# Performance work log

Measured on AMD Instinct MI355X. Metric: run time of the kernel, lower is better.

Reference implementation:

```python
import jax, jax.numpy as jnp
import numpy as np

B, S, H, DK = 4, 2048, 16, 64
D = H * DK  # d_model = 1024


def setup_inputs() -> dict:
    key = jax.random.key(0)
    ks = jax.random.split(key, 11)
    s = 1.0 / np.sqrt(D)
    return {
        "query": jax.random.normal(ks[0], (B, S, D), dtype=jnp.float32),
        "value": jax.random.normal(ks[1], (B, S, D), dtype=jnp.float32),
        "key": jax.random.normal(ks[2], (B, S, D), dtype=jnp.float32),
        "Wq": jax.random.normal(ks[3], (D, D), dtype=jnp.float32) * s,
        "bq": jnp.zeros((D,), dtype=jnp.float32),
        "Wk": jax.random.normal(ks[4], (D, D), dtype=jnp.float32) * s,
        "bk": jnp.zeros((D,), dtype=jnp.float32),
        "Wv": jax.random.normal(ks[5], (D, D), dtype=jnp.float32) * s,
        "bv": jnp.zeros((D,), dtype=jnp.float32),
        "Wo": jax.random.normal(ks[6], (D, D), dtype=jnp.float32) * s,
        "bo": jnp.zeros((D,), dtype=jnp.float32),
    }


def _split_heads(x):
    # [B, S, D] -> [B, H, S, DK]
    return x.reshape(B, -1, H, DK).transpose(0, 2, 1, 3)


def reference(query, value, key, Wq, bq, Wk, bk, Wv, bv, Wo, bo):
    q = _split_heads(query @ Wq + bq)
    k = _split_heads(key @ Wk + bk)
    v = _split_heads(value @ Wv + bv)
    logits = jnp.einsum("bhqd,bhkd->bhqk", q, k) / jnp.sqrt(jnp.float32(DK))
    attn = jax.nn.softmax(logits, axis=-1)
    out = jnp.einsum("bhqk,bhkd->bhqd", attn, v)  # [B, H, S, DK]
    out = out.transpose(0, 2, 1, 3).reshape(B, -1, D)
    return out @ Wo + bo
```

## Files before the change

kernel.cpp:

```cpp
#include <hip/hip_runtime.h>

typedef unsigned short u16;
typedef __attribute__((ext_vector_type(4))) short short4v;
typedef __attribute__((ext_vector_type(8))) short short8;
typedef __attribute__((ext_vector_type(4))) float f32x4;

#define MB_ (1024 * 1024)

__device__ __forceinline__ u16 f2bf(float f) {
  union { float f; unsigned int u; } v; v.f = f;
  unsigned int r = (v.u + 0x7FFFu + ((v.u >> 16) & 1u)) >> 16;
  return (u16)r;
}

__device__ __forceinline__ void async16(const void* g, void* l) {
  __builtin_amdgcn_global_load_lds((__attribute__((address_space(1))) void*)g,
                                   (__attribute__((address_space(3))) void*)l, 16, 0, 0);
}

__device__ __forceinline__ f32x4 mfma32(short8 a, short8 b, f32x4 c) {
  return __builtin_amdgcn_mfma_f32_16x16x32_bf16(a, b, c, 0, 0, 0);
}

__global__ void cvt_x(const float* __restrict__ a, const float* __restrict__ b,
                      const float* __restrict__ c, u16* __restrict__ oa,
                      u16* __restrict__ ob, u16* __restrict__ oc) {
  const float* s = blockIdx.y == 0 ? a : (blockIdx.y == 1 ? b : c);
  u16* d = blockIdx.y == 0 ? oa : (blockIdx.y == 1 ? ob : oc);
  size_t i = ((size_t)blockIdx.x * 256 + threadIdx.x) * 4;
  float4 f = *(const float4*)&s[i];
  ushort4 o;
  o.x = f2bf(f.x); o.y = f2bf(f.y); o.z = f2bf(f.z); o.w = f2bf(f.w);
  *(ushort4*)&d[i] = o;
}

__global__ void wtrans(const float* __restrict__ w0, const float* __restrict__ w1,
                       const float* __restrict__ w2, const float* __restrict__ w3,
                       u16* __restrict__ o0, u16* __restrict__ o1,
                       u16* __restrict__ o2, u16* __restrict__ o3) {
  const int z = blockIdx.z;
  const float* in = z == 0 ? w0 : (z == 1 ? w1 : (z == 2 ? w2 : w3));
  u16* out = z == 0 ? o0 : (z == 1 ? o1 : (z == 2 ? o2 : o3));
  __shared__ float tile[32][33];
  const int bx = blockIdx.x * 32, by = blockIdx.y * 32;
  for (int i = threadIdx.y; i < 32; i += 8)
    tile[i][threadIdx.x] = in[(size_t)(by + i) * 1024 + bx + threadIdx.x];
  __syncthreads();
  for (int i = threadIdx.y; i < 32; i += 8)
    out[(size_t)(bx + i) * 1024 + by + threadIdx.x] = f2bf(tile[threadIdx.x][i]);
}

template <int MODE>
__device__ __forceinline__ void gemm_body(const u16* __restrict__ A, const u16* __restrict__ Bt,
                                          const float* __restrict__ bias, float alpha,
                                          void* __restrict__ outp) {
  __shared__ __align__(16) u16 As[128 * 32];
  __shared__ __align__(16) u16 Bs[128 * 32];
  const int t = threadIdx.x, wave = t >> 6, lane = t & 63;
  const int m0 = blockIdx.y * 128, n0 = blockIdx.x * 128;
  const int wm = (wave >> 1) * 64, wn = (wave & 1) * 64;
  const int lrow = lane >> 2, lcol = (lane & 3) * 8;
  f32x4 acc[4][4] = {};
  for (int k0 = 0; k0 < 1024; k0 += 32) {
    __syncthreads();
#pragma unroll
    for (int c = 0; c < 2; ++c) {
      const int chunk = wave * 2 + c;
      const int row = chunk * 16 + lrow;
      async16(&A[(size_t)(m0 + row) * 1024 + k0 + lcol], &As[chunk * 512]);
      async16(&Bt[(size_t)(n0 + row) * 1024 + k0 + lcol], &Bs[chunk * 512]);
    }
    __syncthreads();
    short8 af[4], bf[4];
#pragma unroll
    for (int mb = 0; mb < 4; ++mb)
      af[mb] = *(const short8*)&As[(wm + mb * 16 + (lane & 15)) * 32 + (lane >> 4) * 8];
#pragma unroll
    for (int nb = 0; nb < 4; ++nb)
      bf[nb] = *(const short8*)&Bs[(wn + nb * 16 + (lane & 15)) * 32 + (lane >> 4) * 8];
#pragma unroll
    for (int mb = 0; mb < 4; ++mb)
#pragma unroll
      for (int nb = 0; nb < 4; ++nb)
        acc[mb][nb] = mfma32(af[mb], bf[nb], acc[mb][nb]);
  }
#pragma unroll
  for (int mb = 0; mb < 4; ++mb)
#pragma unroll
    for (int nb = 0; nb < 4; ++nb) {
      const int n = n0 + wn + nb * 16 + (lane & 15);
      const float bn = bias[n];
      if (MODE == 2) {
        const int h = n >> 6, d = n & 63;
        const int mbase = m0 + wm + mb * 16 + (lane >> 4) * 4;
        const int b = mbase >> 11, s = mbase & 2047;
        ushort4 pk;
        pk.x = f2bf(acc[mb][nb][0] + bn);
        pk.y = f2bf(acc[mb][nb][1] + bn);
        pk.z = f2bf(acc[mb][nb][2] + bn);
        pk.w = f2bf(acc[mb][nb][3] + bn);
        *(ushort4*)&((u16*)outp)[(size_t)((b * 16 + h) * 64 + d) * 2048 + s] = pk;
      } else {
#pragma unroll
        for (int r = 0; r < 4; ++r) {
          const int m = m0 + wm + mb * 16 + (lane >> 4) * 4 + r;
          const float v = (acc[mb][nb][r] + bn) * alpha;
          if (MODE == 1) {
            const int b = m >> 11, s = m & 2047, h = n >> 6, d = n & 63;
            ((u16*)outp)[(size_t)((b * 16 + h) * 2048 + s) * 64 + d] = f2bf(v);
          } else {
            ((float*)outp)[(size_t)m * 1024 + n] = v;
          }
        }
      }
    }
}

__global__ __launch_bounds__(256, 2) void gemm_projqk(
    const u16* xq, const u16* xk, const u16* wq, const u16* wk,
    const float* bq, const float* bk, u16* oq, u16* ok, float aq) {
  const int z = blockIdx.z;
  gemm_body<1>(z == 0 ? xq : xk, z == 0 ? wq : wk, z == 0 ? bq : bk,
               z == 0 ? aq : 1.0f, z == 0 ? (void*)oq : (void*)ok);
}

__global__ __launch_bounds__(256, 2) void gemm_projv(const u16* xv, const u16* wv,
                                                     const float* bv, u16* ov) {
  gemm_body<2>(xv, wv, bv, 1.0f, ov);
}

__global__ __launch_bounds__(256, 2) void gemm_out(const u16* A, const u16* Bt,
                                                   const float* bias, float* o) {
  gemm_body<0>(A, Bt, bias, 1.0f, o);
}

__global__ __launch_bounds__(256, 4) void flash_attn(const u16* __restrict__ Q,
                                                     const u16* __restrict__ K,
                                                     const u16* __restrict__ Vt,
                                                     u16* __restrict__ O) {
  __shared__ __align__(16) u16 lds[2 * 64 * 64];
  u16* Ks = lds;
  u16* Vs = lds + 4096;
  const int t = threadIdx.x, wave = t >> 6, lane = t & 63;
  const int quad = lane >> 4, q15 = lane & 15, sw = q15 & 7;
  const int bh = blockIdx.y, q0 = blockIdx.x * 128;
  const u16* Qb = Q + (size_t)bh * 2048 * 64;
  const u16* Kb = K + (size_t)bh * 2048 * 64;
  const u16* Vb = Vt + (size_t)bh * 64 * 2048;
  const int qrA = q0 + wave * 32 + q15, qrB = qrA + 16;
  const short8 qf00 = *(const short8*)&Qb[(size_t)qrA * 64 + quad * 8];
  const short8 qf01 = *(const short8*)&Qb[(size_t)qrA * 64 + 32 + quad * 8];
  const short8 qf10 = *(const short8*)&Qb[(size_t)qrB * 64 + quad * 8];
  const short8 qf11 = *(const short8*)&Qb[(size_t)qrB * 64 + 32 + quad * 8];
  f32x4 oacc0[4] = {}, oacc1[4] = {};
  float l0 = 0.f, l1 = 0.f;
  for (int kc = 0; kc < 2048; kc += 64) {
    __syncthreads();
#pragma unroll
    for (int c = 0; c < 2; ++c) {
      const int i = wave * 2 + c;
      const int row = i * 8 + (lane >> 3);
      const int ch = (lane & 7) ^ (row & 7);
      async16(&Kb[(size_t)(kc + row) * 64 + ch * 8], &Ks[i * 512]);
      async16(&Vb[(size_t)row * 2048 + kc + ch * 8], &Vs[i * 512]);
    }
    __syncthreads();
    short4v pk0[4], pk1[4];
#pragma unroll
    for (int ma = 0; ma < 4; ++ma) {
      const int rowo = (ma * 16 + q15) * 64;
      const short8 k0 = *(const short8*)&Ks[rowo + ((quad ^ sw) * 8)];
      const short8 k1 = *(const short8*)&Ks[rowo + (((4 + quad) ^ sw) * 8)];
      f32x4 s0 = {}, s1 = {};
      s0 = mfma32(k0, qf00, s0); s0 = mfma32(k1, qf01, s0);
      s1 = mfma32(k0, qf10, s1); s1 = mfma32(k1, qf11, s1);
      short4v a, b;
#pragma unroll
      for (int r = 0; r < 4; ++r) {
        const float p0 = __builtin_exp2f(s0[r]);
        const float p1 = __builtin_exp2f(s1[r]);
        l0 += p0; l1 += p1;
        a[r] = (short)f2bf(p0); b[r] = (short)f2bf(p1);
      }
      pk0[ma] = a; pk1[ma] = b;
    }
#pragma unroll
    for (int mb = 0; mb < 4; ++mb) {
      const int vrow = (mb * 16 + q15) * 64;
#pragma unroll
      for (int kb = 0; kb < 4; ++kb) {
        const int pos = (((kb * 2 + (quad >> 1)) ^ sw) * 8) + (quad & 1) * 4;
        const short4v vf = *(const short4v*)&Vs[vrow + pos];
        oacc0[mb] = __builtin_amdgcn_mfma_f32_16x16x16bf16_1k(vf, pk0[kb], oacc0[mb], 0, 0, 0);
        oacc1[mb] = __builtin_amdgcn_mfma_f32_16x16x16bf16_1k(vf, pk1[kb], oacc1[mb], 0, 0, 0);
      }
    }
  }
  l0 += __shfl_xor(l0, 16); l0 += __shfl_xor(l0, 32);
  l1 += __shfl_xor(l1, 16); l1 += __shfl_xor(l1, 32);
  const float inv0 = 1.f / l0, inv1 = 1.f / l1;
  __syncthreads();
  u16* Es = lds + wave * 2048;
#pragma unroll
  for (int mb = 0; mb < 4; ++mb) {
    const int posc = ((mb * 2 + (quad >> 1)) ^ sw) * 8 + (quad & 1) * 4;
#pragma unroll
    for (int r = 0; r < 4; ++r) {
      Es[q15 * 64 + posc + r] = f2bf(oacc0[mb][r] * inv0);
      Es[(16 + q15) * 64 + posc + r] = f2bf(oacc1[mb][r] * inv1);
    }
  }
  __syncthreads();
  const int b = bh >> 4, h = bh & 15;
#pragma unroll
  for (int pass = 0; pass < 4; ++pass) {
    const int rw = pass * 8 + (lane >> 3);
    const int j = lane & 7;
    const short8 val = *(const short8*)&Es[rw * 64 + ((j ^ (rw & 7)) * 8)];
    *(short8*)&O[((size_t)(b * 2048 + q0 + wave * 32 + rw)) * 1024 + h * 64 + j * 8] = val;
  }
}

extern "C" void kernel_launch(void* const* d_in, const int* in_sizes, int n_in,
                              void* d_out, int out_size, void* d_ws, size_t ws_size,
                              hipStream_t stream) {
  const float* q_in = (const float*)d_in[0];
  const float* v_in = (const float*)d_in[1];
  const float* k_in = (const float*)d_in[2];
  const float* Wq = (const float*)d_in[3];
  const float* bq = (const float*)d_in[4];
  const float* Wk = (const float*)d_in[5];
  const float* bk = (const float*)d_in[6];
  const float* Wv = (const float*)d_in[7];
  const float* bv = (const float*)d_in[8];
  const float* Wo = (const float*)d_in[9];
  const float* bo = (const float*)d_in[10];
  float* out = (float*)d_out;
  char* ws = (char*)d_ws;

  u16* xq = (u16*)(ws);
  u16* xk = (u16*)(ws + 16 * (size_t)MB_);
  u16* xv = (u16*)(ws + 32 * (size_t)MB_);
  u16* wqT = (u16*)(ws + 48 * (size_t)MB_);
  u16* wkT = (u16*)(ws + 50 * (size_t)MB_);
  u16* wvT = (u16*)(ws + 52 * (size_t)MB_);
  u16* woT = (u16*)(ws + 54 * (size_t)MB_);
  u16* qb = (u16*)(ws + 56 * (size_t)MB_);
  u16* kb = (u16*)(ws + 72 * (size_t)MB_);
  u16* vb = (u16*)(ws + 88 * (size_t)MB_);
  u16* ao = xq;

  const float aq = 0.125f * 1.44269504088896340736f;

  cvt_x<<<dim3(8192, 3), 256, 0, stream>>>(q_in, k_in, v_in, xq, xk, xv);
  wtrans<<<dim3(32, 32, 4), dim3(32, 8), 0, stream>>>(Wq, Wk, Wv, Wo, wqT, wkT, wvT, woT);
  gemm_projqk<<<dim3(8, 64, 2), 256, 0, stream>>>(xq, xk, wqT, wkT, bq, bk, qb, kb, aq);
  gemm_projv<<<dim3(8, 64), 256, 0, stream>>>(xv, wvT, bv, vb);
  flash_attn<<<dim3(16, 64), 256, 0, stream>>>(qb, kb, vb, ao);
  gemm_out<<<dim3(8, 64), 256, 0, stream>>>(ao, woT, bo, out);
}
```

Baseline: 392.3 us.

## Merge QKV projections, halve flash-attention query tile, use packed bf16 conversion

Merges the Q/K and V projection GEMMs into one launch with a runtime mode switch. Halves the flash-attention query tile from 128 to 64 rows per block (16 per wave), doubling the grid and raising launch-bounds occupancy to 8. It also replaces scalar bf16 rounding with a packed perm-based conversion that rounds half-up instead of to-nearest-even. The smaller tile means each K/V chunk loaded into LDS is reused by half as many query rows, so global and LDS traffic per unit of work rises in exchange for more parallelism.

```diff
diff --git a/kernel.cpp b/kernel.cpp
--- a/kernel.cpp
+++ b/kernel.cpp
@@ -11,6 +11,11 @@
   union { float f; unsigned int u; } v; v.f = f;
   unsigned int r = (v.u + 0x7FFFu + ((v.u >> 16) & 1u)) >> 16;
   return (u16)r;
+}
+
+__device__ __forceinline__ unsigned int pkbf(float a, float b) {
+  union { float f; unsigned int u; } x, y; x.f = a; y.f = b;
+  return __builtin_amdgcn_perm(y.u + 0x8000u, x.u + 0x8000u, 0x07060302u);
 }
 
 __device__ __forceinline__ void async16(const void* g, void* l) {
@@ -50,10 +55,9 @@
     out[(size_t)(bx + i) * 1024 + by + threadIdx.x] = f2bf(tile[threadIdx.x][i]);
 }
 
-template <int MODE>
 __device__ __forceinline__ void gemm_body(const u16* __restrict__ A, const u16* __restrict__ Bt,
                                           const float* __restrict__ bias, float alpha,
-                                          void* __restrict__ outp) {
+                                          int mode, void* __restrict__ outp) {
   __shared__ __align__(16) u16 As[128 * 32];
   __shared__ __align__(16) u16 Bs[128 * 32];
   const int t = threadIdx.x, wave = t >> 6, lane = t & 63;
@@ -90,51 +94,51 @@
     for (int nb = 0; nb < 4; ++nb) {
       const int n = n0 + wn + nb * 16 + (lane & 15);
       const float bn = bias[n];
-      if (MODE == 2) {
+      if (mode == 2) {
         const int h = n >> 6, d = n & 63;
         const int mbase = m0 + wm + mb * 16 + (lane >> 4) * 4;
         const int b = mbase >> 11, s = mbase & 2047;
-        ushort4 pk;
-        pk.x = f2bf(acc[mb][nb][0] + bn);
-        pk.y = f2bf(acc[mb][nb][1] + bn);
-        pk.z = f2bf(acc[mb][nb][2] + bn);
-        pk.w = f2bf(acc[mb][nb][3] + bn);
-        *(ushort4*)&((u16*)outp)[(size_t)((b * 16 + h) * 64 + d) * 2048 + s] = pk;
-      } else {
+        union { unsigned int u[2]; ushort4 s4; } pk;
+        pk.u[0] = pkbf(acc[mb][nb][0] + bn, acc[mb][nb][1] + bn);
+        pk.u[1] = pkbf(acc[mb][nb][2] + bn, acc[mb][nb][3] + bn);
+        *(ushort4*)&((u16*)outp)[(size_t)((b * 16 + h) * 64 + d) * 2048 + s] = pk.s4;
+      } else if (mode == 1) {
 #pragma unroll
         for (int r = 0; r < 4; ++r) {
           const int m = m0 + wm + mb * 16 + (lane >> 4) * 4 + r;
-          const float v = (acc[mb][nb][r] + bn) * alpha;
-          if (MODE == 1) {
-            const int b = m >> 11, s = m & 2047, h = n >> 6, d = n & 63;
-            ((u16*)outp)[(size_t)((b * 16 + h) * 2048 + s) * 64 + d] = f2bf(v);
-          } else {
-            ((float*)outp)[(size_t)m * 1024 + n] = v;
-          }
+          const int b = m >> 11, s = m & 2047, h = n >> 6, d = n & 63;
+          ((u16*)outp)[(size_t)((b * 16 + h) * 2048 + s) * 64 + d] =
+              (u16)(pkbf(acc[mb][nb][r] * alpha + bn * alpha, 0.f) & 0xFFFFu);
+        }
+      } else {
+#pragma unroll
+        for (int r = 0; r < 4; ++r) {
+          const int m = m0 + wm + mb * 16 + (lane >> 4) * 4 + r;
+          ((float*)outp)[(size_t)m * 1024 + n] = acc[mb][nb][r] + bn;
         }
       }
     }
 }
 
-__global__ __launch_bounds__(256, 2) void gemm_projqk(
-    const u16* xq, const u16* xk, const u16* wq, const u16* wk,
-    const float* bq, const float* bk, u16* oq, u16* ok, float aq) {
+__global__ __launch_bounds__(256, 2) void gemm_proj(
+    const u16* xq, const u16* xk, const u16* xv,
+    const u16* wq, const u16* wk, const u16* wv,
+    const float* bq, const float* bk, const float* bv,
+    u16* oq, u16* ok, u16* ov, float aq) {
   const int z = blockIdx.z;
-  gemm_body<1>(z == 0 ? xq : xk, z == 0 ? wq : wk, z == 0 ? bq : bk,
-               z == 0 ? aq : 1.0f, z == 0 ? (void*)oq : (void*)ok);
-}
-
-__global__ __launch_bounds__(256, 2) void gemm_projv(const u16* xv, const u16* wv,
-                                                     const float* bv, u16* ov) {
-  gemm_body<2>(xv, wv, bv, 1.0f, ov);
+  const u16* A = z == 0 ? xq : (z == 1 ? xk : xv);
+  const u16* B = z == 0 ? wq : (z == 1 ? wk : wv);
+  const float* bi = z == 0 ? bq : (z == 1 ? bk : bv);
+  void* o = z == 0 ? (void*)oq : (z == 1 ? (void*)ok : (void*)ov);
+  gemm_body(A, B, bi, z == 0 ? aq : 1.0f, z == 2 ? 2 : 1, o);
 }
 
 __global__ __launch_bounds__(256, 2) void gemm_out(const u16* A, const u16* Bt,
                                                    const float* bias, float* o) {
-  gemm_body<0>(A, Bt, bias, 1.0f, o);
-}
-
-__global__ __launch_bounds__(256, 4) void flash_attn(const u16* __restrict__ Q,
+  gemm_body(A, Bt, bias, 1.0f, 0, o);
+}
+
+__global__ __launch_bounds__(256, 8) void flash_attn(const u16* __restrict__ Q,
                                                      const u16* __restrict__ K,
                                                      const u16* __restrict__ Vt,
                                                      u16* __restrict__ O) {
@@ -143,17 +147,15 @@
   u16* Vs = lds + 4096;
   const int t = threadIdx.x, wave = t >> 6, lane = t & 63;
   const int quad = lane >> 4, q15 = lane & 15, sw = q15 & 7;
-  const int bh = blockIdx.y, q0 = blockIdx.x * 128;
+  const int bh = blockIdx.y, q0 = blockIdx.x * 64;
   const u16* Qb = Q + (size_t)bh * 2048 * 64;
   const u16* Kb = K + (size_t)bh * 2048 * 64;
   const u16* Vb = Vt + (size_t)bh * 64 * 2048;
-  const int qrA = q0 + wave * 32 + q15, qrB = qrA + 16;
-  const short8 qf00 = *(const short8*)&Qb[(size_t)qrA * 64 + quad * 8];
-  const short8 qf01 = *(const short8*)&Qb[(size_t)qrA * 64 + 32 + quad * 8];
-  const short8 qf10 = *(const short8*)&Qb[(size_t)qrB * 64 + quad * 8];
-  const short8 qf11 = *(const short8*)&Qb[(size_t)qrB * 64 + 32 + quad * 8];
-  f32x4 oacc0[4] = {}, oacc1[4] = {};
-  float l0 = 0.f, l1 = 0.f;
+  const int qr = q0 + wave * 16 + q15;
+  const short8 qf0 = *(const short8*)&Qb[(size_t)qr * 64 + quad * 8];
+  const short8 qf1 = *(const short8*)&Qb[(size_t)qr * 64 + 32 + quad * 8];
+  f32x4 oacc[4] = {};
+  float l = 0.f;
   for (int kc = 0; kc < 2048; kc += 64) {
     __syncthreads();
 #pragma unroll
@@ -165,25 +167,26 @@
       async16(&Vb[(size_t)row * 2048 + kc + ch * 8], &Vs[i * 512]);
     }
     __syncthreads();
-    short4v pk0[4], pk1[4];
+    short4v pk[4];
 #pragma unroll
     for (int ma = 0; ma < 4; ++ma) {
       const int rowo = (ma * 16 + q15) * 64;
       const short8 k0 = *(const short8*)&Ks[rowo + ((quad ^ sw) * 8)];
       const short8 k1 = *(const short8*)&Ks[rowo + (((4 + quad) ^ sw) * 8)];
-      f32x4 s0 = {}, s1 = {};
-      s0 = mfma32(k0, qf00, s0); s0 = mfma32(k1, qf01, s0);
-      s1 = mfma32(k0, qf10, s1); s1 = mfma32(k1, qf11, s1);
-      short4v a, b;
-#pragma unroll
-      for (int r = 0; r < 4; ++r) {
-        const float p0 = __builtin_exp2f(s0[r]);
-        const float p1 = __builtin_exp2f(s1[r]);
-        l0 += p0; l1 += p1;
-        a[r] = (short)f2bf(p0); b[r] = (short)f2bf(p1);
-      }
-      pk0[ma] = a; pk1[ma] = b;
-    }
+      f32x4 s0 = {};
+      s0 = mfma32(k0, qf0, s0);
+      s0 = mfma32(k1, qf1, s0);
+      float p0 = __builtin_exp2f(s0[0]);
+      float p1 = __builtin_exp2f(s0[1]);
+      float p2 = __builtin_exp2f(s0[2]);
+      float p3 = __builtin_exp2f(s0[3]);
+      l += (p0 + p1) + (p2 + p3);
+      union { unsigned int u[2]; short4v s4; } pq;
+      pq.u[0] = pkbf(p0, p1);
+      pq.u[1] = pkbf(p2, p3);
+      pk[ma] = pq.s4;
+    }
+#if __has_builtin(__builtin_amdgcn_mfma_f32_16x16x16bf16_1k)
 #pragma unroll
     for (int mb = 0; mb < 4; ++mb) {
       const int vrow = (mb * 16 + q15) * 64;
@@ -191,33 +194,49 @@
       for (int kb = 0; kb < 4; ++kb) {
         const int pos = (((kb * 2 + (quad >> 1)) ^ sw) * 8) + (quad & 1) * 4;
         const short4v vf = *(const short4v*)&Vs[vrow + pos];
-        oacc0[mb] = __builtin_amdgcn_mfma_f32_16x16x16bf16_1k(vf, pk0[kb], oacc0[mb], 0, 0, 0);
-        oacc1[mb] = __builtin_amdgcn_mfma_f32_16x16x16bf16_1k(vf, pk1[kb], oacc1[mb], 0, 0, 0);
+        oacc[mb] = __builtin_amdgcn_mfma_f32_16x16x16bf16_1k(vf, pk[kb], oacc[mb], 0, 0, 0);
       }
     }
-  }
-  l0 += __shfl_xor(l0, 16); l0 += __shfl_xor(l0, 32);
-  l1 += __shfl_xor(l1, 16); l1 += __shfl_xor(l1, 32);
-  const float inv0 = 1.f / l0, inv1 = 1.f / l1;
+#else
+    {
+      const int* pi = (const int*)&pk[0];
+#pragma unroll
+      for (int kb2 = 0; kb2 < 2; ++kb2) {
+        const int lo = quad < 2 ? pi[kb2 * 4 + 0] : pi[kb2 * 4 + 2];
+        const int hi = quad < 2 ? pi[kb2 * 4 + 1] : pi[kb2 * 4 + 3];
+        const int src = (2 * (quad & 1)) * 16 + q15;
+        union { int i[4]; short8 s; } u;
+        u.i[0] = __shfl(lo, src);      u.i[1] = __shfl(hi, src);
+        u.i[2] = __shfl(lo, src + 16); u.i[3] = __shfl(hi, src + 16);
+#pragma unroll
+        for (int mb = 0; mb < 4; ++mb) {
+          const short8 vf8 = *(const short8*)&Vs[(mb * 16 + q15) * 64 + (((kb2 * 4 + quad) ^ sw) * 8)];
+          oacc[mb] = mfma32(vf8, u.s, oacc[mb]);
+        }
+      }
+    }
+#endif
+  }
+  l += __shfl_xor(l, 16);
+  l += __shfl_xor(l, 32);
+  const float inv = 1.f / l;
   __syncthreads();
-  u16* Es = lds + wave * 2048;
+  u16* Es = lds + wave * 1024;
 #pragma unroll
   for (int mb = 0; mb < 4; ++mb) {
     const int posc = ((mb * 2 + (quad >> 1)) ^ sw) * 8 + (quad & 1) * 4;
-#pragma unroll
-    for (int r = 0; r < 4; ++r) {
-      Es[q15 * 64 + posc + r] = f2bf(oacc0[mb][r] * inv0);
-      Es[(16 + q15) * 64 + posc + r] = f2bf(oacc1[mb][r] * inv1);
-    }
-  }
-  __syncthreads();
+    union { unsigned int u[2]; ushort4 s4; } pq;
+    pq.u[0] = pkbf(oacc[mb][0] * inv, oacc[mb][1] * inv);
+    pq.u[1] = pkbf(oacc[mb][2] * inv, oacc[mb][3] * inv);
+    *(ushort4*)&Es[q15 * 64 + posc] = pq.s4;
+  }
   const int b = bh >> 4, h = bh & 15;
 #pragma unroll
-  for (int pass = 0; pass < 4; ++pass) {
+  for (int pass = 0; pass < 2; ++pass) {
     const int rw = pass * 8 + (lane >> 3);
     const int j = lane & 7;
     const short8 val = *(const short8*)&Es[rw * 64 + ((j ^ (rw & 7)) * 8)];
-    *(short8*)&O[((size_t)(b * 2048 + q0 + wave * 32 + rw)) * 1024 + h * 64 + j * 8] = val;
+    *(short8*)&O[((size_t)(b * 2048 + q0 + wave * 16 + rw)) * 1024 + h * 64 + j * 8] = val;
   }
 }
 
@@ -254,8 +273,7 @@
 
   cvt_x<<<dim3(8192, 3), 256, 0, stream>>>(q_in, k_in, v_in, xq, xk, xv);
   wtrans<<<dim3(32, 32, 4), dim3(32, 8), 0, stream>>>(Wq, Wk, Wv, Wo, wqT, wkT, wvT, woT);
-  gemm_projqk<<<dim3(8, 64, 2), 256, 0, stream>>>(xq, xk, wqT, wkT, bq, bk, qb, kb, aq);
-  gemm_projv<<<dim3(8, 64), 256, 0, stream>>>(xv, wvT, bv, vb);
-  flash_attn<<<dim3(16, 64), 256, 0, stream>>>(qb, kb, vb, ao);
+  gemm_proj<<<dim3(8, 64, 3), 256, 0, stream>>>(xq, xk, xv, wqT, wkT, wvT, bq, bk, bv, qb, kb, vb, aq);
+  flash_attn<<<dim3(32, 64), 256, 0, stream>>>(qb, kb, vb, ao);
   gemm_out<<<dim3(8, 64), 256, 0, stream>>>(ao, woT, bo, out);
 }
```

Measured after the change: 400.7 us. 1.02x slower.
